# Optimization experiments

Measured on AMD Instinct MI355X. Metric: run time of the kernel, lower is better.

Reference implementation:

```python
import jax, jax.numpy as jnp
import numpy as np

N_NODES = 50000
N_EDGES = 800000


def _spmm(edge_row, edge_col, edge_w, h):
    # sparse adj @ h via gather + segment-sum: adj[r,c] = edge_w
    msgs = edge_w[:, None] * h[edge_col]          # [E, D] gather
    return jax.ops.segment_sum(msgs, edge_row, num_segments=N_NODES)


def setup_inputs() -> dict:
    key = jax.random.key(0)
    ks = jax.random.split(key, 8)
    x = jax.random.normal(ks[0], (N_NODES, 256), dtype=jnp.float32)
    edge_row = jax.random.randint(ks[1], (N_EDGES,), 0, N_NODES, dtype=jnp.int32)
    edge_col = jax.random.randint(ks[2], (N_EDGES,), 0, N_NODES, dtype=jnp.int32)
    edge_w = jax.random.uniform(ks[3], (N_EDGES,), dtype=jnp.float32)
    W1 = jax.random.normal(ks[4], (256, 128), dtype=jnp.float32) * 0.06
    b1 = jnp.zeros((128,), dtype=jnp.float32)
    W2 = jax.random.normal(ks[5], (128, 32), dtype=jnp.float32) * 0.09
    b2 = jnp.zeros((32,), dtype=jnp.float32)
    return {"x": x, "edge_row": edge_row, "edge_col": edge_col,
            "edge_w": edge_w, "W1": W1, "b1": b1, "W2": W2, "b2": b2}


def reference(x, edge_row, edge_col, edge_w, W1, b1, W2, b2):
    # Layer 1: support = X @ W1 ; out = relu(A @ support + b1)
    # (dropout is identity in eval mode)
    h = jax.nn.relu(_spmm(edge_row, edge_col, edge_w, x @ W1) + b1)
    # Layer 2
    out = jax.nn.relu(_spmm(edge_row, edge_col, edge_w, h @ W2) + b2)
    return out
```

## Files before the change

### kernel.cpp

```cpp
#include <hip/hip_runtime.h>

#define N_NODES 50000
#define N_EDGES 800000
#define D0 256
#define D1 128
#define D2 32
#define CAP 64
#define SCAT_BLOCKS 391
#define G1_BLOCKS 782

typedef unsigned short u16;
typedef unsigned int   u32;
typedef __attribute__((ext_vector_type(8))) short bf16x8;
typedef __attribute__((ext_vector_type(4))) float f32x4;

__device__ inline u32 bf16rne(float f) {
    union { float f; u32 u; } c; c.f = f;
    return (c.u + 0x7FFFu + ((c.u >> 16) & 1u)) >> 16;
}
__device__ inline float bfhi(u32 v) {
    union { u32 u; float f; } c; c.u = v & 0xFFFF0000u; return c.f;
}
__device__ inline float bflo(u32 v) {
    union { u32 u; float f; } c; c.u = v << 16; return c.f;
}

__global__ __launch_bounds__(256) void front_kernel(const float* __restrict__ W1,
                                                    u16* __restrict__ Bsw1,
                                                    const float* __restrict__ W2,
                                                    u16* __restrict__ Bsw2) {
    const int bid = blockIdx.x;
    if (bid < 16) {
        const int id = bid * 256 + threadIdx.x;
        const int lane = id & 63;
        const int t    = (id >> 6) & 7;
        const int ks   = id >> 9;
        const int n     = t * 16 + (lane & 15);
        const int kbase = ks * 32 + (lane >> 4) * 8;
        u32 v[8];
        #pragma unroll
        for (int j = 0; j < 8; ++j) v[j] = bf16rne(W1[(kbase + j) * D1 + n]);
        uint4 w;
        w.x = v[0] | (v[1] << 16);
        w.y = v[2] | (v[3] << 16);
        w.z = v[4] | (v[5] << 16);
        w.w = v[6] | (v[7] << 16);
        ((uint4*)Bsw1)[id] = w;
    } else {
        const int id = (bid - 16) * 256 + threadIdx.x;
        const int lane = id & 63;
        const int t    = (id >> 6) & 1;
        const int ks   = id >> 7;
        const int n     = t * 16 + (lane & 15);
        const int kbase = ks * 32 + (lane >> 4) * 8;
        u32 v[8];
        #pragma unroll
        for (int j = 0; j < 8; ++j) v[j] = bf16rne(W2[(kbase + j) * D2 + n]);
        uint4 w;
        w.x = v[0] | (v[1] << 16);
        w.y = v[2] | (v[3] << 16);
        w.z = v[4] | (v[5] << 16);
        w.w = v[6] | (v[7] << 16);
        ((uint4*)Bsw2)[id] = w;
    }
}

__global__ __launch_bounds__(256) void mid_kernel(const float* __restrict__ x,
                                                  const u16* __restrict__ Bsw1,
                                                  u16* __restrict__ s1b,
                                                  const int* __restrict__ erow,
                                                  const int* __restrict__ ecol,
                                                  const float* __restrict__ ew,
                                                  int* __restrict__ cnt,
                                                  u32* __restrict__ eg) {
    const int bid = blockIdx.x;
    if (bid < G1_BLOCKS) {
        const int lane = threadIdx.x & 63;
        const int wave = threadIdx.x >> 6;
        const int rowbase = bid * 64 + wave * 16;
        const int m    = lane & 15;
        const int quad = lane >> 4;
        int arow = rowbase + m;
        if (arow >= N_NODES) arow = N_NODES - 1;
        const float* aptr = x + (size_t)arow * D0 + quad * 8;

        f32x4 acc[8];
        #pragma unroll
        for (int t = 0; t < 8; ++t) acc[t] = (f32x4){0.f, 0.f, 0.f, 0.f};

        #pragma unroll
        for (int ks = 0; ks < 8; ++ks) {
            const float4 f0 = *(const float4*)(aptr + ks * 32);
            const float4 f1 = *(const float4*)(aptr + ks * 32 + 4);
            bf16x8 a;
            a[0] = (short)bf16rne(f0.x); a[1] = (short)bf16rne(f0.y);
            a[2] = (short)bf16rne(f0.z); a[3] = (short)bf16rne(f0.w);
            a[4] = (short)bf16rne(f1.x); a[5] = (short)bf16rne(f1.y);
            a[6] = (short)bf16rne(f1.z); a[7] = (short)bf16rne(f1.w);
            const u16* bp = Bsw1 + ((size_t)(ks * 8) * 64 + lane) * 8;
            #pragma unroll
            for (int t = 0; t < 8; ++t) {
                const bf16x8 b = *(const bf16x8*)(bp + (size_t)t * 64 * 8);
                acc[t] = __builtin_amdgcn_mfma_f32_16x16x32_bf16(a, b, acc[t], 0, 0, 0);
            }
        }
        const int orow = rowbase + quad * 4;
        #pragma unroll
        for (int r = 0; r < 4; ++r) {
            const int row = orow + r;
            if (row < N_NODES) {
                u16* op = s1b + (size_t)row * D1 + m;
                #pragma unroll
                for (int t = 0; t < 8; ++t) op[t * 16] = (u16)bf16rne(acc[t][r]);
            }
        }
    } else {
        const int base = (bid - G1_BLOCKS) * 2048 + threadIdx.x;
        int  rows[8], cols[8];
        float ws[8];
        bool valid[8];
        #pragma unroll
        for (int k = 0; k < 8; ++k) {
            const int e = base + k * 256;
            valid[k] = e < N_EDGES;
            if (valid[k]) { rows[k] = erow[e]; cols[k] = ecol[e]; ws[k] = ew[e]; }
        }
        #pragma unroll
        for (int k = 0; k < 8; ++k) {
            if (valid[k]) {
                const int p = atomicAdd(&cnt[rows[k]], 1);
                if (p < CAP)
                    eg[(size_t)rows[k] * CAP + p] = (u32)cols[k] | (bf16rne(ws[k]) << 16);
            }
        }
    }
}

__global__ __launch_bounds__(256) void spmm_csr128_kernel(const int* __restrict__ cnt,
                                                          const u32* __restrict__ eg,
                                                          const u16* __restrict__ src,
                                                          const float* __restrict__ bias,
                                                          u16* __restrict__ dst) {
    const int lane = threadIdx.x;
    const int row  = blockIdx.x * 8 + threadIdx.y;
    if (row >= N_NODES) return;
    int len = cnt[row];
    if (len > CAP) len = CAP;
    const u32* ep = eg + (size_t)row * CAP;
    float4 a0 = {0.f,0.f,0.f,0.f}, a1 = {0.f,0.f,0.f,0.f};
    float4 a2 = {0.f,0.f,0.f,0.f}, a3 = {0.f,0.f,0.f,0.f};
    int j = 0;
    for (; j + 3 < len; j += 4) {
        const uint4 e4 = *(const uint4*)(ep + j);
        const uint2 v0 = ((const uint2*)(src + (size_t)(e4.x & 0xFFFFu) * D1))[lane];
        const uint2 v1 = ((const uint2*)(src + (size_t)(e4.y & 0xFFFFu) * D1))[lane];
        const uint2 v2 = ((const uint2*)(src + (size_t)(e4.z & 0xFFFFu) * D1))[lane];
        const uint2 v3 = ((const uint2*)(src + (size_t)(e4.w & 0xFFFFu) * D1))[lane];
        const float w0 = bfhi(e4.x), w1 = bfhi(e4.y), w2 = bfhi(e4.z), w3 = bfhi(e4.w);
        a0.x += w0 * bflo(v0.x); a0.y += w0 * bfhi(v0.x);
        a0.z += w0 * bflo(v0.y); a0.w += w0 * bfhi(v0.y);
        a1.x += w1 * bflo(v1.x); a1.y += w1 * bfhi(v1.x);
        a1.z += w1 * bflo(v1.y); a1.w += w1 * bfhi(v1.y);
        a2.x += w2 * bflo(v2.x); a2.y += w2 * bfhi(v2.x);
        a2.z += w2 * bflo(v2.y); a2.w += w2 * bfhi(v2.y);
        a3.x += w3 * bflo(v3.x); a3.y += w3 * bfhi(v3.x);
        a3.z += w3 * bflo(v3.y); a3.w += w3 * bfhi(v3.y);
    }
    for (; j < len; ++j) {
        const u32 e0 = ep[j];
        const float w0 = bfhi(e0);
        const uint2 v0 = ((const uint2*)(src + (size_t)(e0 & 0xFFFFu) * D1))[lane];
        a0.x += w0 * bflo(v0.x); a0.y += w0 * bfhi(v0.x);
        a0.z += w0 * bflo(v0.y); a0.w += w0 * bfhi(v0.y);
    }
    const float4 b4 = ((const float4*)bias)[lane];
    float rx = a0.x + a1.x + a2.x + a3.x + b4.x; rx = rx > 0.f ? rx : 0.f;
    float ry = a0.y + a1.y + a2.y + a3.y + b4.y; ry = ry > 0.f ? ry : 0.f;
    float rz = a0.z + a1.z + a2.z + a3.z + b4.z; rz = rz > 0.f ? rz : 0.f;
    float rw = a0.w + a1.w + a2.w + a3.w + b4.w; rw = rw > 0.f ? rw : 0.f;
    uint2 o;
    o.x = bf16rne(rx) | (bf16rne(ry) << 16);
    o.y = bf16rne(rz) | (bf16rne(rw) << 16);
    ((uint2*)(dst + (size_t)row * D1))[lane] = o;
}

__global__ __launch_bounds__(256) void gemm2_mfma_kernel(const u16* __restrict__ hb,
                                                         const u16* __restrict__ Bsw2,
                                                         u16* __restrict__ s2b) {
    const int lane = threadIdx.x & 63;
    const int wave = threadIdx.x >> 6;
    const int rowbase = blockIdx.x * 64 + wave * 16;
    const int m    = lane & 15;
    const int quad = lane >> 4;
    int arow = rowbase + m;
    if (arow >= N_NODES) arow = N_NODES - 1;
    const u16* aptr = hb + (size_t)arow * D1 + quad * 8;

    f32x4 acc0 = (f32x4){0.f,0.f,0.f,0.f};
    f32x4 acc1 = (f32x4){0.f,0.f,0.f,0.f};

    #pragma unroll
    for (int ks = 0; ks < 4; ++ks) {
        const bf16x8 a = *(const bf16x8*)(aptr + ks * 32);
        const u16* bp = Bsw2 + ((size_t)(ks * 2) * 64 + lane) * 8;
        const bf16x8 b0 = *(const bf16x8*)(bp);
        const bf16x8 b1 = *(const bf16x8*)(bp + (size_t)64 * 8);
        acc0 = __builtin_amdgcn_mfma_f32_16x16x32_bf16(a, b0, acc0, 0, 0, 0);
        acc1 = __builtin_amdgcn_mfma_f32_16x16x32_bf16(a, b1, acc1, 0, 0, 0);
    }
    const int orow = rowbase + quad * 4;
    #pragma unroll
    for (int r = 0; r < 4; ++r) {
        const int row = orow + r;
        if (row < N_NODES) {
            u16* op = s2b + (size_t)row * D2 + m;
            op[0]  = (u16)bf16rne(acc0[r]);
            op[16] = (u16)bf16rne(acc1[r]);
        }
    }
}

__global__ __launch_bounds__(256) void spmm_csr32_kernel(const int* __restrict__ cnt,
                                                         const u32* __restrict__ eg,
                                                         const u16* __restrict__ src,
                                                         const float* __restrict__ bias,
                                                         float* __restrict__ out) {
    const int lane = threadIdx.x;
    const int row  = blockIdx.x * 16 + threadIdx.y;
    if (row >= N_NODES) return;
    int len = cnt[row];
    if (len > CAP) len = CAP;
    const u32* ep = eg + (size_t)row * CAP;
    float ax0=0.f, ay0=0.f, ax1=0.f, ay1=0.f, ax2=0.f, ay2=0.f, ax3=0.f, ay3=0.f;
    int j = 0;
    for (; j + 3 < len; j += 4) {
        const uint4 e4 = *(const uint4*)(ep + j);
        const u32 v0 = ((const u32*)(src + (size_t)(e4.x & 0xFFFFu) * D2))[lane];
        const u32 v1 = ((const u32*)(src + (size_t)(e4.y & 0xFFFFu) * D2))[lane];
        const u32 v2 = ((const u32*)(src + (size_t)(e4.z & 0xFFFFu) * D2))[lane];
        const u32 v3 = ((const u32*)(src + (size_t)(e4.w & 0xFFFFu) * D2))[lane];
        const float w0 = bfhi(e4.x), w1 = bfhi(e4.y), w2 = bfhi(e4.z), w3 = bfhi(e4.w);
        ax0 += w0 * bflo(v0); ay0 += w0 * bfhi(v0);
        ax1 += w1 * bflo(v1); ay1 += w1 * bfhi(v1);
        ax2 += w2 * bflo(v2); ay2 += w2 * bfhi(v2);
        ax3 += w3 * bflo(v3); ay3 += w3 * bfhi(v3);
    }
    for (; j < len; ++j) {
        const u32 e0 = ep[j];
        const u32 v0 = ((const u32*)(src + (size_t)(e0 & 0xFFFFu) * D2))[lane];
        const float w0 = bfhi(e0);
        ax0 += w0 * bflo(v0); ay0 += w0 * bfhi(v0);
    }
    const float2 b2v = ((const float2*)bias)[lane];
    float vx = ax0 + ax1 + ax2 + ax3 + b2v.x; vx = vx > 0.f ? vx : 0.f;
    float vy = ay0 + ay1 + ay2 + ay3 + b2v.y; vy = vy > 0.f ? vy : 0.f;
    ((float2*)(out + (size_t)row * D2))[lane] = make_float2(vx, vy);
}

extern "C" void kernel_launch(void* const* d_in, const int* in_sizes, int n_in,
                              void* d_out, int out_size, void* d_ws, size_t ws_size,
                              hipStream_t stream) {
    const float* x    = (const float*)d_in[0];
    const int*   erow = (const int*)  d_in[1];
    const int*   ecol = (const int*)  d_in[2];
    const float* ew   = (const float*)d_in[3];
    const float* W1   = (const float*)d_in[4];
    const float* b1   = (const float*)d_in[5];
    const float* W2   = (const float*)d_in[6];
    const float* b2   = (const float*)d_in[7];
    float* out = (float*)d_out;

    int* cnt   = (int*)d_ws;
    u32* eg    = (u32*)(cnt + N_NODES);
    u16* Bsw1  = (u16*)(eg + (size_t)N_NODES * CAP);
    u16* Bsw2  = Bsw1 + 8 * 8 * 64 * 8;
    u16* s1b   = Bsw2 + 4 * 2 * 64 * 8;
    u16* hb    = s1b + (size_t)N_NODES * D1;
    u16* s2b   = hb + (size_t)N_NODES * D1;

    hipMemsetAsync(cnt, 0, N_NODES * sizeof(int), stream);
    front_kernel<<<18, 256, 0, stream>>>(W1, Bsw1, W2, Bsw2);
    mid_kernel<<<G1_BLOCKS + SCAT_BLOCKS, 256, 0, stream>>>(
        x, Bsw1, s1b, erow, ecol, ew, cnt, eg);
    spmm_csr128_kernel<<<(N_NODES + 7) / 8, dim3(32, 8), 0, stream>>>(cnt, eg, s1b, b1, hb);
    gemm2_mfma_kernel<<<(N_NODES + 63) / 64, 256, 0, stream>>>(hb, Bsw2, s2b);
    spmm_csr32_kernel<<<(N_NODES + 15) / 16, dim3(16, 16), 0, stream>>>(cnt, eg, s2b, b2, out);
}
```

Measured before the change: 210.6 us.

## Replace global-atomic edge scatter with two-pass bucketed binning through shared memory

The per-edge global atomicAdd on per-row counters is replaced by a two-level scheme. First, blocks histogram edges into 391 buckets of 128 rows each in LDS, reserve space with one global atomic per bucket, and write packed edges to a bucket buffer that reuses the hb region. A new bucket_kernel then builds each bucket's per-row lists in shared memory and writes eg and cnt with coalesced vector stores. This cuts random global atomics and scattered writes, at the cost of an extra kernel launch, an extra pass over the edges, and a per-bucket cap of 3072 edges that could overflow on skewed inputs.

```diff
diff --git a/kernel.cpp b/kernel.cpp
--- a/kernel.cpp
+++ b/kernel.cpp
@@ -6,11 +6,15 @@
 #define D1 128
 #define D2 32
 #define CAP 64
-#define SCAT_BLOCKS 391
+#define NB 391
+#define BCAP 3072
+#define EB 8192
+#define P1_BLOCKS 98
 #define G1_BLOCKS 782
 
 typedef unsigned short u16;
 typedef unsigned int   u32;
+typedef unsigned long long u64;
 typedef __attribute__((ext_vector_type(8))) short bf16x8;
 typedef __attribute__((ext_vector_type(4))) float f32x4;
 
@@ -71,13 +75,47 @@
                                                   const int* __restrict__ erow,
                                                   const int* __restrict__ ecol,
                                                   const float* __restrict__ ew,
-                                                  int* __restrict__ cnt,
-                                                  u32* __restrict__ eg) {
+                                                  u32* __restrict__ bcur,
+                                                  u64* __restrict__ ebuf) {
     const int bid = blockIdx.x;
-    if (bid < G1_BLOCKS) {
+    if (bid < P1_BLOCKS) {
+        __shared__ u32 hist[NB];
+        __shared__ u32 lbase[NB];
+        for (int i = threadIdx.x; i < NB; i += 256) hist[i] = 0;
+        __syncthreads();
+        const int ebase = bid * EB;
+        #pragma unroll 4
+        for (int k = 0; k < EB / 256; ++k) {
+            const int e = ebase + k * 256 + threadIdx.x;
+            if (e < N_EDGES) atomicAdd(&hist[erow[e] >> 7], 1u);
+        }
+        __syncthreads();
+        for (int i = threadIdx.x; i < NB; i += 256) {
+            const u32 h = hist[i];
+            lbase[i] = h ? atomicAdd(&bcur[i], h) : 0u;
+            hist[i] = 0;
+        }
+        __syncthreads();
+        #pragma unroll 2
+        for (int k = 0; k < EB / 256; ++k) {
+            const int e = ebase + k * 256 + threadIdx.x;
+            if (e < N_EDGES) {
+                const int r = erow[e];
+                const int c = ecol[e];
+                const float w = ew[e];
+                const int b = r >> 7;
+                const u32 lr = atomicAdd(&hist[b], 1u);
+                const u32 pos = lbase[b] + lr;
+                if (pos < BCAP)
+                    ebuf[(size_t)b * BCAP + pos] =
+                        (u64)(u32)c | ((u64)(u32)(r & 127) << 16) | ((u64)bf16rne(w) << 32);
+            }
+        }
+    } else {
+        const int gb   = bid - P1_BLOCKS;
         const int lane = threadIdx.x & 63;
         const int wave = threadIdx.x >> 6;
-        const int rowbase = bid * 64 + wave * 16;
+        const int rowbase = gb * 64 + wave * 16;
         const int m    = lane & 15;
         const int quad = lane >> 4;
         int arow = rowbase + m;
@@ -114,26 +152,38 @@
                 for (int t = 0; t < 8; ++t) op[t * 16] = (u16)bf16rne(acc[t][r]);
             }
         }
-    } else {
-        const int base = (bid - G1_BLOCKS) * 2048 + threadIdx.x;
-        int  rows[8], cols[8];
-        float ws[8];
-        bool valid[8];
-        #pragma unroll
-        for (int k = 0; k < 8; ++k) {
-            const int e = base + k * 256;
-            valid[k] = e < N_EDGES;
-            if (valid[k]) { rows[k] = erow[e]; cols[k] = ecol[e]; ws[k] = ew[e]; }
-        }
-        #pragma unroll
-        for (int k = 0; k < 8; ++k) {
-            if (valid[k]) {
-                const int p = atomicAdd(&cnt[rows[k]], 1);
-                if (p < CAP)
-                    eg[(size_t)rows[k] * CAP + p] = (u32)cols[k] | (bf16rne(ws[k]) << 16);
-            }
-        }
-    }
+    }
+}
+
+__global__ __launch_bounds__(256) void bucket_kernel(const u32* __restrict__ bcur,
+                                                     const u64* __restrict__ ebuf,
+                                                     int* __restrict__ cnt,
+                                                     u32* __restrict__ eg) {
+    const int b = blockIdx.x;
+    __shared__ u32 seg[128 * CAP];
+    __shared__ u32 lcnt[128];
+    for (int i = threadIdx.x; i < 128; i += 256) lcnt[i] = 0;
+    __syncthreads();
+    int n = (int)bcur[b];
+    if (n > BCAP) n = BCAP;
+    const u64* ep = ebuf + (size_t)b * BCAP;
+    for (int i = threadIdx.x; i < n; i += 256) {
+        const u64 e = ep[i];
+        const u32 c  = (u32)(e & 0xFFFFu);
+        const u32 lr = (u32)((e >> 16) & 0x7Fu);
+        const u32 w  = (u32)(e >> 32);
+        const u32 p = atomicAdd(&lcnt[lr], 1u);
+        if (p < CAP)
+            seg[lr * CAP + p] = c | (w << 16);
+    }
+    __syncthreads();
+    const int rows = min(128, N_NODES - b * 128);
+    for (int i = threadIdx.x; i < rows; i += 256)
+        cnt[b * 128 + i] = (int)min(lcnt[i], (u32)CAP);
+    u32* dst = eg + (size_t)b * 128 * CAP;
+    const int nvec = rows * (CAP / 4);
+    for (int i = threadIdx.x; i < nvec; i += 256)
+        ((uint4*)dst)[i] = ((const uint4*)seg)[i];
 }
 
 __global__ __launch_bounds__(256) void spmm_csr128_kernel(const int* __restrict__ cnt,
@@ -271,17 +321,20 @@
     float* out = (float*)d_out;
 
     int* cnt   = (int*)d_ws;
-    u32* eg    = (u32*)(cnt + N_NODES);
+    u32* bcur  = (u32*)(cnt + N_NODES);
+    u32* eg    = (u32*)(bcur + 512);
     u16* Bsw1  = (u16*)(eg + (size_t)N_NODES * CAP);
     u16* Bsw2  = Bsw1 + 8 * 8 * 64 * 8;
     u16* s1b   = Bsw2 + 4 * 2 * 64 * 8;
     u16* hb    = s1b + (size_t)N_NODES * D1;
     u16* s2b   = hb + (size_t)N_NODES * D1;
-
-    hipMemsetAsync(cnt, 0, N_NODES * sizeof(int), stream);
+    u64* ebuf  = (u64*)hb;
+
+    hipMemsetAsync(bcur, 0, 512 * sizeof(u32), stream);
     front_kernel<<<18, 256, 0, stream>>>(W1, Bsw1, W2, Bsw2);
-    mid_kernel<<<G1_BLOCKS + SCAT_BLOCKS, 256, 0, stream>>>(
-        x, Bsw1, s1b, erow, ecol, ew, cnt, eg);
+    mid_kernel<<<P1_BLOCKS + G1_BLOCKS, 256, 0, stream>>>(
+        x, Bsw1, s1b, erow, ecol, ew, bcur, ebuf);
+    bucket_kernel<<<NB, 256, 0, stream>>>(bcur, ebuf, cnt, eg);
     spmm_csr128_kernel<<<(N_NODES + 7) / 8, dim3(32, 8), 0, stream>>>(cnt, eg, s1b, b1, hb);
     gemm2_mfma_kernel<<<(N_NODES + 63) / 64, 256, 0, stream>>>(hb, Bsw2, s2b);
     spmm_csr32_kernel<<<(N_NODES + 15) / 16, dim3(16, 16), 0, stream>>>(cnt, eg, s2b, b2, out);
```

New measurement: 200.9 us. -4.6%, faster.
